# Kernel optimization log

Measured on AMD Instinct MI355X. Metric: run time of the kernel, lower is better.

Reference implementation:

```python
import jax, jax.numpy as jnp
import numpy as np

EMB = 512
H = 8
DK = EMB // H          # 64
MAX_SEQ = 768
TOPK = MAX_SEQ // 2    # 384


def setup_inputs() -> dict:
    key = jax.random.key(0)
    ks = jax.random.split(key, 16)
    B, S, E = 1, MAX_SEQ, EMB

    def w(k, shape):
        return jax.random.normal(k, shape, dtype=jnp.float32) * 0.02

    return {
        "x": jax.random.normal(ks[0], (B, S, E), dtype=jnp.float32),
        # main attention projections (Linear weights stored as (in, out))
        "Wq": w(ks[1], (E, E)), "bq": w(ks[2], (E,)),
        "Wk": w(ks[3], (E, E)), "bk": w(ks[4], (E,)),
        "Wv": w(ks[5], (E, E)), "bv": w(ks[6], (E,)),
        "Wo": w(ks[7], (E, E)), "bo": w(ks[8], (E,)),
        # indexer projections: wq -> (E, H*DK)=(E,E), wk -> (E, DK), weights_proj -> (E, H)
        "iq_W": w(ks[9], (E, H * DK)), "iq_b": w(ks[10], (H * DK,)),
        "ik_W": w(ks[11], (E, DK)),    "ik_b": w(ks[12], (DK,)),
        "wp_W": w(ks[13], (E, H)),     "wp_b": w(ks[14], (H,)),
    }


def reference(x, Wq, bq, Wk, bk, Wv, bv, Wo, bo, iq_W, iq_b, ik_W, ik_b, wp_W, wp_b):
    B, S, E = x.shape
    scaling = 1.0 / np.sqrt(DK)

    def split_heads(z):  # (B,S,E) -> (B,H,S,DK)
        return z.reshape(B, S, H, DK).transpose(0, 2, 1, 3)

    Q = split_heads(x @ Wq + bq)
    K = split_heads(x @ Wk + bk)
    V = split_heads(x @ Wv + bv)

    # --- indexer: per-token relevance scores ---
    q_idx = (x @ iq_W + iq_b).reshape(B, S, H, DK).transpose(0, 2, 1, 3)  # (B,H,S,DK)
    k_idx = x @ ik_W + ik_b                                               # (B,S,DK)
    w_idx = x @ wp_W + wp_b                                               # (B,S,H)
    score = jax.nn.relu(jnp.einsum('bhsd,btd->bhst', q_idx, k_idx))       # (B,H,S,S)
    indexer_score = jnp.einsum('bhst,bsh->bst', score, w_idx)             # (B,S,S)

    # --- top-k selection (set-equivalent to argpartition in the original) ---
    topk_idx = jax.lax.top_k(indexer_score, TOPK)[1]                      # (B,S,TOPK) int32

    # --- gather sparse K/V per query token ---
    def gather_b(Zb, idxb):  # Zb:(H,S,DK), idxb:(S,TOPK) -> (H,S,TOPK,DK)
        return Zb[:, idxb, :]
    K_s = jax.vmap(gather_b)(K, topk_idx)  # (B,H,S,TOPK,DK)
    V_s = jax.vmap(gather_b)(V, topk_idx)  # (B,H,S,TOPK,DK)

    # --- sparse attention over selected tokens ---
    sc = jnp.einsum('bhsd,bhskd->bhsk', Q, K_s) * scaling  # (B,H,S,TOPK)
    wts = jax.nn.softmax(sc, axis=-1)
    attn = jnp.einsum('bhsk,bhskd->bhsd', wts, V_s)        # (B,H,S,DK)

    out = attn.transpose(0, 2, 1, 3).reshape(B, S, E) @ Wo + bo
    return out
```

## Files before the change

kernel.cpp:

```cpp
#include <hip/hip_runtime.h>
#include <hip/hip_bf16.h>
#include <math.h>

#define S 768
#define E 512
#define H 8
#define DK 64
#define TOPK 384

typedef short bf16x8 __attribute__((ext_vector_type(8)));
typedef float f32x4 __attribute__((ext_vector_type(4)));

__device__ __forceinline__ unsigned short f2bf(float x) {
  unsigned u = __float_as_uint(x);
  unsigned r = u + 0x7FFFu + ((u >> 16) & 1u);
  return (unsigned short)(r >> 16);
}
__device__ __forceinline__ float bf2f(unsigned short h) {
  return __uint_as_float(((unsigned)h) << 16);
}
__device__ __forceinline__ void split1(float x, unsigned short& h, unsigned short& l) {
  h = f2bf(x);
  l = f2bf(x - bf2f(h));
}

__device__ __forceinline__ void mfma3(f32x4& d, bf16x8 ah, bf16x8 al,
                                      bf16x8 bh, bf16x8 bl) {
  d = __builtin_amdgcn_mfma_f32_16x16x32_bf16(ah, bh, d, 0, 0, 0);
  d = __builtin_amdgcn_mfma_f32_16x16x32_bf16(ah, bl, d, 0, 0, 0);
  d = __builtin_amdgcn_mfma_f32_16x16x32_bf16(al, bh, d, 0, 0, 0);
}
__device__ __forceinline__ void mfma2(f32x4& d, bf16x8 ah, bf16x8 al, bf16x8 bh) {
  d = __builtin_amdgcn_mfma_f32_16x16x32_bf16(ah, bh, d, 0, 0, 0);
  d = __builtin_amdgcn_mfma_f32_16x16x32_bf16(al, bh, d, 0, 0, 0);
}

__device__ __forceinline__ bf16x8 ldfrag(const unsigned short* p) {
  return *reinterpret_cast<const bf16x8*>(p);
}

struct PrepTab {
  const float* src[8];
  unsigned short* hi[8];
  unsigned short* lo[8];
};

__global__ __launch_bounds__(256) void prep_kernel(PrepTab t) {
  const int seg = blockIdx.z;
  const int rows = (seg == 0) ? 768 : 512;
  const int cols = (seg == 5) ? 64 : ((seg == 6) ? 8 : 512);
  const int tx = (seg == 6) ? 2 : ((cols + 31) >> 5);
  const int ty = rows >> 5;
  if ((int)blockIdx.x >= tx || (int)blockIdx.y >= ty) return;
  const int r0 = blockIdx.y * 32, c0 = blockIdx.x * 32;
  const int tid = threadIdx.x;
  const int rl = tid >> 3, c4 = (tid & 7) << 2;
  const float* src = t.src[seg];
  if (seg == 0) {
    float4 v = *(const float4*)(src + (size_t)(r0 + rl) * cols + c0 + c4);
    unsigned short h[4], l[4];
    split1(v.x, h[0], l[0]); split1(v.y, h[1], l[1]);
    split1(v.z, h[2], l[2]); split1(v.w, h[3], l[3]);
    size_t off = (size_t)(r0 + rl) * cols + c0 + c4;
    *(ushort4*)(t.hi[seg] + off) = make_ushort4(h[0], h[1], h[2], h[3]);
    *(ushort4*)(t.lo[seg] + off) = make_ushort4(l[0], l[1], l[2], l[3]);
  } else {
    __shared__ float ts[32][33];
    #pragma unroll
    for (int j = 0; j < 4; ++j) {
      int c = c4 + j;
      ts[rl][c] = (c0 + c < cols) ? src[(size_t)(r0 + rl) * cols + c0 + c] : 0.0f;
    }
    __syncthreads();
    float v0 = ts[c4 + 0][rl], v1 = ts[c4 + 1][rl];
    float v2 = ts[c4 + 2][rl], v3 = ts[c4 + 3][rl];
    unsigned short h[4], l[4];
    split1(v0, h[0], l[0]); split1(v1, h[1], l[1]);
    split1(v2, h[2], l[2]); split1(v3, h[3], l[3]);
    size_t off = (size_t)(c0 + rl) * 512 + r0 + c4;
    *(ushort4*)(t.hi[seg] + off) = make_ushort4(h[0], h[1], h[2], h[3]);
    *(ushort4*)(t.lo[seg] + off) = make_ushort4(l[0], l[1], l[2], l[3]);
  }
}

struct ProjTab {
  const unsigned short* whi[6];
  const unsigned short* wlo[6];
  const float* bias[6];
};

__global__ __launch_bounds__(256) void proj_mfma_kernel(
    const unsigned short* __restrict__ Xhi, const unsigned short* __restrict__ Xlo,
    ProjTab pt,
    unsigned short* __restrict__ Qhi, unsigned short* __restrict__ Qlo,
    unsigned short* __restrict__ Khi, unsigned short* __restrict__ Klo,
    unsigned short* __restrict__ VThi,
    unsigned short* __restrict__ QIhi, unsigned short* __restrict__ QIlo,
    unsigned short* __restrict__ KIhi, unsigned short* __restrict__ KIlo,
    float* __restrict__ WI) {
  __shared__ __align__(16) unsigned short Ah[64][72];
  __shared__ __align__(16) unsigned short Al[64][72];
  __shared__ __align__(16) unsigned short Bh[64][72];
  __shared__ __align__(16) unsigned short Bl[64][72];
  const int bx = blockIdx.x;
  int seg, nt;
  if (bx < 32) { seg = bx >> 3; nt = bx & 7; }
  else         { seg = 4 + (bx - 32); nt = 0; }
  const int m0 = blockIdx.y * 64;
  const int n0 = nt * 64;
  const int tid = threadIdx.x;
  const int lane = tid & 63;
  const int wave = tid >> 6;
  const int mq = (wave >> 1) << 5;
  const int nq = (wave & 1) << 5;
  const int l15 = lane & 15;
  const int q8 = (lane >> 4) << 3;
  const int q4 = (lane >> 4) << 2;
  const unsigned short* Whi = pt.whi[seg];
  const unsigned short* Wlo = pt.wlo[seg];

  const int mm0 = tid >> 3,          kc0 = (tid & 7) << 3;
  const int mm1 = (tid + 256) >> 3,  kc1 = ((tid + 256) & 7) << 3;
  const size_t ga0 = (size_t)(m0 + mm0) * 512 + kc0;
  const size_t gb0 = (size_t)(n0 + mm0) * 512 + kc0;
  const size_t ga1 = (size_t)(m0 + mm1) * 512 + kc1;
  const size_t gb1 = (size_t)(n0 + mm1) * 512 + kc1;

  bf16x8 rah0 = ldfrag(Xhi + ga0), ral0 = ldfrag(Xlo + ga0);
  bf16x8 rbh0 = ldfrag(Whi + gb0), rbl0 = ldfrag(Wlo + gb0);
  bf16x8 rah1 = ldfrag(Xhi + ga1), ral1 = ldfrag(Xlo + ga1);
  bf16x8 rbh1 = ldfrag(Whi + gb1), rbl1 = ldfrag(Wlo + gb1);

  f32x4 acc[2][2] = {};
  for (int cc = 0; cc < 8; ++cc) {
    *(bf16x8*)&Ah[mm0][kc0] = rah0;
    *(bf16x8*)&Al[mm0][kc0] = ral0;
    *(bf16x8*)&Bh[mm0][kc0] = rbh0;
    *(bf16x8*)&Bl[mm0][kc0] = rbl0;
    *(bf16x8*)&Ah[mm1][kc1] = rah1;
    *(bf16x8*)&Al[mm1][kc1] = ral1;
    *(bf16x8*)&Bh[mm1][kc1] = rbh1;
    *(bf16x8*)&Bl[mm1][kc1] = rbl1;
    if (cc < 7) {
      const size_t o = (size_t)(cc + 1) << 6;
      rah0 = ldfrag(Xhi + ga0 + o); ral0 = ldfrag(Xlo + ga0 + o);
      rbh0 = ldfrag(Whi + gb0 + o); rbl0 = ldfrag(Wlo + gb0 + o);
      rah1 = ldfrag(Xhi + ga1 + o); ral1 = ldfrag(Xlo + ga1 + o);
      rbh1 = ldfrag(Whi + gb1 + o); rbl1 = ldfrag(Wlo + gb1 + o);
    }
    __syncthreads();
    #pragma unroll
    for (int ki = 0; ki < 64; ki += 32) {
      const int kk = ki + q8;
      bf16x8 ah0 = *(const bf16x8*)&Ah[mq + l15][kk];
      bf16x8 al0 = *(const bf16x8*)&Al[mq + l15][kk];
      bf16x8 ah1 = *(const bf16x8*)&Ah[mq + 16 + l15][kk];
      bf16x8 al1 = *(const bf16x8*)&Al[mq + 16 + l15][kk];
      bf16x8 bh0 = *(const bf16x8*)&Bh[nq + l15][kk];
      bf16x8 bl0 = *(const bf16x8*)&Bl[nq + l15][kk];
      bf16x8 bh1 = *(const bf16x8*)&Bh[nq + 16 + l15][kk];
      bf16x8 bl1 = *(const bf16x8*)&Bl[nq + 16 + l15][kk];
      mfma3(acc[0][0], ah0, al0, bh0, bl0);
      mfma3(acc[0][1], ah0, al0, bh1, bl1);
      mfma3(acc[1][0], ah1, al1, bh0, bl0);
      mfma3(acc[1][1], ah1, al1, bh1, bl1);
    }
    __syncthreads();
  }

  const float* bias = pt.bias[seg];
  #pragma unroll
  for (int ntt = 0; ntt < 2; ++ntt) {
    const int nloc = n0 + nq + ntt * 16 + l15;
    const float bv = (seg == 5 && nloc >= 8) ? 0.0f : bias[nloc];
    #pragma unroll
    for (int mt = 0; mt < 2; ++mt) {
      #pragma unroll
      for (int r = 0; r < 4; ++r) {
        const int m = m0 + mq + mt * 16 + q4 + r;
        const float v = acc[mt][ntt][r] + bv;
        unsigned short h16, l16;
        if (seg == 0) {
          split1(v, h16, l16);
          Qhi[(size_t)m * 512 + nloc] = h16;
          Qlo[(size_t)m * 512 + nloc] = l16;
        } else if (seg == 1) {
          const int hh = nloc >> 6, dd = nloc & 63;
          split1(v, h16, l16);
          Khi[((size_t)hh * S + m) * 64 + dd] = h16;
          Klo[((size_t)hh * S + m) * 64 + dd] = l16;
        } else if (seg == 2) {
          VThi[((size_t)(nloc >> 6) * 64 + (nloc & 63)) * S + m] = f2bf(v);
        } else if (seg == 3) {
          split1(v, h16, l16);
          QIhi[(size_t)m * 512 + nloc] = h16;
          QIlo[(size_t)m * 512 + nloc] = l16;
        } else if (seg == 4) {
          split1(v, h16, l16);
          KIhi[(size_t)m * 64 + nloc] = h16;
          KIlo[(size_t)m * 64 + nloc] = l16;
        } else {
          if (nloc < 8) WI[(size_t)m * 8 + nloc] = v;
        }
      }
    }
  }
}

__global__ __launch_bounds__(256) void indexer_mfma_kernel(
    const unsigned short* __restrict__ QIhi, const unsigned short* __restrict__ QIlo,
    const unsigned short* __restrict__ KIhi, const unsigned short* __restrict__ KIlo,
    const float* __restrict__ WI, float* __restrict__ ISC) {
  __shared__ __align__(16) unsigned short Qh[32][136];
  __shared__ __align__(16) unsigned short Ql[32][136];
  __shared__ float wis[32][8];
  const int s0 = blockIdx.y * 32, t0 = blockIdx.x * 64;
  const int tid = threadIdx.x;
  const int lane = tid & 63;
  const int wave = tid >> 6;
  const int mq = (wave >> 1) << 4;
  const int nqb = (wave & 1) << 5;
  const int l15 = lane & 15;
  const int q8 = (lane >> 4) << 3;
  const int q4 = (lane >> 4) << 2;
  wis[tid >> 3][tid & 7] = WI[(size_t)(s0 + (tid >> 3)) * 8 + (tid & 7)];

  const size_t brow0 = (size_t)(t0 + nqb + l15) * 64;
  const size_t brow1 = (size_t)(t0 + nqb + 16 + l15) * 64;
  bf16x8 kfh[2][2], kfl[2][2];
  #pragma unroll
  for (int kk = 0; kk < 2; ++kk) {
    const int kb = kk * 32 + q8;
    kfh[kk][0] = ldfrag(KIhi + brow0 + kb);
    kfl[kk][0] = ldfrag(KIlo + brow0 + kb);
    kfh[kk][1] = ldfrag(KIhi + brow1 + kb);
    kfl[kk][1] = ldfrag(KIlo + brow1 + kb);
  }

  const int smm = tid >> 3;
  const int skc = (tid & 7) << 4;
  const size_t qbase = (size_t)(s0 + smm) * 512 + skc;
  bf16x8 rq0 = ldfrag(QIhi + qbase);
  bf16x8 rq1 = ldfrag(QIhi + qbase + 8);
  bf16x8 rq2 = ldfrag(QIlo + qbase);
  bf16x8 rq3 = ldfrag(QIlo + qbase + 8);

  float accI[2][4] = {};
  for (int hp = 0; hp < 4; ++hp) {
    __syncthreads();
    *(bf16x8*)&Qh[smm][skc]     = rq0;
    *(bf16x8*)&Qh[smm][skc + 8] = rq1;
    *(bf16x8*)&Ql[smm][skc]     = rq2;
    *(bf16x8*)&Ql[smm][skc + 8] = rq3;
    if (hp < 3) {
      const size_t g = qbase + (size_t)(hp + 1) * 128;
      rq0 = ldfrag(QIhi + g);
      rq1 = ldfrag(QIhi + g + 8);
      rq2 = ldfrag(QIlo + g);
      rq3 = ldfrag(QIlo + g + 8);
    }
    __syncthreads();
    #pragma unroll
    for (int hh = 0; hh < 2; ++hh) {
      const int h = hp * 2 + hh;
      f32x4 d[2] = {};
      #pragma unroll
      for (int kk = 0; kk < 2; ++kk) {
        const int ka = hh * 64 + kk * 32 + q8;
        bf16x8 ah = *(const bf16x8*)&Qh[mq + l15][ka];
        bf16x8 al = *(const bf16x8*)&Ql[mq + l15][ka];
        mfma3(d[0], ah, al, kfh[kk][0], kfl[kk][0]);
        mfma3(d[1], ah, al, kfh[kk][1], kfl[kk][1]);
      }
      #pragma unroll
      for (int r = 0; r < 4; ++r) {
        const float w = wis[mq + q4 + r][h];
        accI[0][r] = fmaf(fmaxf(d[0][r], 0.0f), w, accI[0][r]);
        accI[1][r] = fmaf(fmaxf(d[1][r], 0.0f), w, accI[1][r]);
      }
    }
  }
  #pragma unroll
  for (int ntt = 0; ntt < 2; ++ntt)
    #pragma unroll
    for (int r = 0; r < 4; ++r)
      ISC[(size_t)(s0 + mq + q4 + r) * S + t0 + nqb + ntt * 16 + l15] = accI[ntt][r];
}

__global__ __launch_bounds__(256) void topk_kernel(
    const float* __restrict__ ISC, unsigned* __restrict__ Mask,
    float* __restrict__ Sum, float* __restrict__ ATTacc) {
  __shared__ unsigned ordv[768];
  __shared__ int hist[256];
  __shared__ int gsum[16];
  __shared__ int wtot[4];
  __shared__ unsigned mw[24];
  __shared__ unsigned sh_prefix;
  __shared__ int sh_R;
  const int s = blockIdx.x;
  const int tid = threadIdx.x;
  for (int i = tid; i < 768; i += 256) {
    float f = ISC[s * 768 + i] + 0.0f;
    unsigned u = __float_as_uint(f);
    ordv[i] = (u & 0x80000000u) ? ~u : (u | 0x80000000u);
  }
  {
    const float4 z4 = {0.0f, 0.0f, 0.0f, 0.0f};
    if (tid < 128) *(float4*)(ATTacc + (size_t)s * 512 + tid * 4) = z4;
  }
  if (tid < 24) mw[tid] = 0u;
  if (tid < H) Sum[tid * S + s] = 0.0f;
  if (tid == 0) { sh_prefix = 0u; sh_R = TOPK; }
  __syncthreads();
  for (int pass = 0; pass < 4; ++pass) {
    const int shift = 24 - pass * 8;
    hist[tid] = 0;
    __syncthreads();
    const unsigned pm = (pass == 0) ? 0u : (0xFFFFFFFFu << (shift + 8));
    const unsigned pref = sh_prefix;
    for (int i = tid; i < 768; i += 256) {
      unsigned o = ordv[i];
      if ((o & pm) == pref) atomicAdd(&hist[(o >> shift) & 255], 1);
    }
    __syncthreads();
    if (tid < 16) {
      int t = 0;
      #pragma unroll
      for (int k = 0; k < 16; ++k) t += hist[tid * 16 + k];
      gsum[tid] = t;
    }
    __syncthreads();
    if (tid == 0) {
      int R = sh_R;
      int G = 0;
      int g = 15;
      for (; g > 0; --g) {
        if (G + gsum[g] >= R) break;
        G += gsum[g];
      }
      int b = 15;
      for (; b > 0; --b) {
        int c = hist[g * 16 + b];
        if (G + c >= R) break;
        G += c;
      }
      sh_prefix = sh_prefix | ((unsigned)(g * 16 + b) << shift);
      sh_R = R - G;
    }
    __syncthreads();
  }
  const unsigned thr = sh_prefix;
  const int need_eq = sh_R;
  const int base = tid * 3;
  unsigned o0 = ordv[base], o1 = ordv[base + 1], o2 = ordv[base + 2];
  int c = (o0 == thr) + (o1 == thr) + (o2 == thr);
  const int lane = tid & 63, wv = tid >> 6;
  int sum = c;
  #pragma unroll
  for (int off = 1; off < 64; off <<= 1) {
    int v = __shfl_up(sum, off);
    if (lane >= off) sum += v;
  }
  if (lane == 63) wtot[wv] = sum;
  __syncthreads();
  int rank = sum - c;
  if (wv > 0) rank += wtot[0];
  if (wv > 1) rank += wtot[1];
  if (wv > 2) rank += wtot[2];
  if (o0 > thr || (o0 == thr && rank < need_eq))
    atomicOr(&mw[base >> 5], 1u << (base & 31));
  if (o0 == thr) ++rank;
  if (o1 > thr || (o1 == thr && rank < need_eq))
    atomicOr(&mw[(base + 1) >> 5], 1u << ((base + 1) & 31));
  if (o1 == thr) ++rank;
  if (o2 > thr || (o2 == thr && rank < need_eq))
    atomicOr(&mw[(base + 2) >> 5], 1u << ((base + 2) & 31));
  __syncthreads();
  if (tid < 24) Mask[s * 24 + tid] = mw[tid];
}

__global__ __launch_bounds__(512) void sattn_kernel(
    const unsigned short* __restrict__ Qhi, const unsigned short* __restrict__ Qlo,
    const unsigned short* __restrict__ Khi, const unsigned short* __restrict__ Klo,
    const unsigned short* __restrict__ VThi,
    const unsigned* __restrict__ Mask, float* __restrict__ ATTacc,
    float* __restrict__ Sum) {
  __shared__ __align__(16) unsigned short Ksh[64][72];
  __shared__ __align__(16) unsigned short Ksl[64][72];
  __shared__ __align__(16) unsigned short Pshi[64][72];
  __shared__ __align__(16) unsigned short Pslo[64][72];
  __shared__ unsigned msk[64][6];
  __shared__ float rsumf[64];
  const int ks = blockIdx.x;
  const int s0 = blockIdx.y * 64;
  const int h  = blockIdx.z;
  const int tid = threadIdx.x;
  const int lane = tid & 63;
  const int wave = tid >> 6;
  const int l15 = lane & 15;
  const int q8 = (lane >> 4) << 3;
  const int q4 = (lane >> 4) << 2;
  const int mq = (wave >> 1) << 4;
  const int nqq = (wave & 1) << 4;
  const int db = (wave & 1) << 5;

  if (tid < 384) msk[tid & 63][tid >> 6] =
      Mask[(size_t)(s0 + (tid & 63)) * 24 + ks * 6 + (tid >> 6)];
  if (tid < 64) rsumf[tid] = 0.0f;

  const size_t qrow = (size_t)(s0 + mq + l15) * 512 + h * 64;
  bf16x8 qh0 = ldfrag(Qhi + qrow + q8);
  bf16x8 ql0 = ldfrag(Qlo + qrow + q8);
  bf16x8 qh1 = ldfrag(Qhi + qrow + 32 + q8);
  bf16x8 ql1 = ldfrag(Qlo + qrow + 32 + q8);

  const int tr = tid >> 3;
  const int kc = (tid & 7) << 3;
  const size_t gkbase = ((size_t)h * S + ks * 192 + tr) * 64 + kc;
  bf16x8 rkh = ldfrag(Khi + gkbase);
  bf16x8 rkl = ldfrag(Klo + gkbase);

  const size_t vb0 = ((size_t)h * 64 + db + l15) * S + ks * 192 + q8;
  bf16x8 v00 = ldfrag(VThi + vb0);
  bf16x8 v01 = ldfrag(VThi + vb0 + 32);
  bf16x8 v10 = ldfrag(VThi + vb0 + (size_t)16 * S);
  bf16x8 v11 = ldfrag(VThi + vb0 + (size_t)16 * S + 32);

  float esum[4] = {0.0f, 0.0f, 0.0f, 0.0f};
  f32x4 oacc[2] = {};
  for (int ct = 0; ct < 3; ++ct) {
    __syncthreads();
    if (ct > 0) {
      #pragma unroll
      for (int kk = 0; kk < 64; kk += 32) {
        bf16x8 pah = *(const bf16x8*)&Pshi[mq + l15][kk + q8];
        bf16x8 pal = *(const bf16x8*)&Pslo[mq + l15][kk + q8];
        mfma2(oacc[0], pah, pal, (kk == 0) ? v00 : v01);
        mfma2(oacc[1], pah, pal, (kk == 0) ? v10 : v11);
      }
      const size_t vo = vb0 + (size_t)ct * 64;
      v00 = ldfrag(VThi + vo);
      v01 = ldfrag(VThi + vo + 32);
      v10 = ldfrag(VThi + vo + (size_t)16 * S);
      v11 = ldfrag(VThi + vo + (size_t)16 * S + 32);
    }
    *(bf16x8*)&Ksh[tr][kc] = rkh;
    *(bf16x8*)&Ksl[tr][kc] = rkl;
    if (ct < 2) {
      rkh = ldfrag(Khi + gkbase + (size_t)(ct + 1) * 4096);
      rkl = ldfrag(Klo + gkbase + (size_t)(ct + 1) * 4096);
    }
    __syncthreads();
    #pragma unroll
    for (int cp = 0; cp < 2; ++cp) {
      const int tcol = nqq + cp * 32;
      f32x4 d = {0.0f, 0.0f, 0.0f, 0.0f};
      bf16x8 bh0 = *(const bf16x8*)&Ksh[tcol + l15][q8];
      bf16x8 bl0 = *(const bf16x8*)&Ksl[tcol + l15][q8];
      bf16x8 bh1 = *(const bf16x8*)&Ksh[tcol + l15][32 + q8];
      bf16x8 bl1 = *(const bf16x8*)&Ksl[tcol + l15][32 + q8];
      mfma3(d, qh0, ql0, bh0, bl0);
      mfma3(d, qh1, ql1, bh1, bl1);
      const int tl = ct * 64 + tcol + l15;
      #pragma unroll
      for (int r = 0; r < 4; ++r) {
        const int srow = mq + q4 + r;
        const unsigned w = msk[srow][tl >> 5];
        float e = ((w >> (tl & 31)) & 1u) ? __expf(d[r] * 0.125f) : 0.0f;
        unsigned short h16, l16;
        split1(e, h16, l16);
        Pshi[srow][tcol + l15] = h16;
        Pslo[srow][tcol + l15] = l16;
        esum[r] += e;
      }
    }
  }
  __syncthreads();
  #pragma unroll
  for (int kk = 0; kk < 64; kk += 32) {
    bf16x8 pah = *(const bf16x8*)&Pshi[mq + l15][kk + q8];
    bf16x8 pal = *(const bf16x8*)&Pslo[mq + l15][kk + q8];
    mfma2(oacc[0], pah, pal, (kk == 0) ? v00 : v01);
    mfma2(oacc[1], pah, pal, (kk == 0) ? v10 : v11);
  }
  #pragma unroll
  for (int dt = 0; dt < 2; ++dt) {
    const int dd = db + dt * 16 + l15;
    #pragma unroll
    for (int r = 0; r < 4; ++r) {
      const int s = s0 + mq + q4 + r;
      atomicAdd(&ATTacc[(size_t)s * E + h * DK + dd], oacc[dt][r]);
    }
  }
  #pragma unroll
  for (int off = 1; off < 16; off <<= 1) {
    esum[0] += __shfl_xor(esum[0], off);
    esum[1] += __shfl_xor(esum[1], off);
    esum[2] += __shfl_xor(esum[2], off);
    esum[3] += __shfl_xor(esum[3], off);
  }
  if (l15 == 0) {
    atomicAdd(&rsumf[q4 + 0 + mq], esum[0]);
    atomicAdd(&rsumf[q4 + 1 + mq], esum[1]);
    atomicAdd(&rsumf[q4 + 2 + mq], esum[2]);
    atomicAdd(&rsumf[q4 + 3 + mq], esum[3]);
  }
  __syncthreads();
  if (tid < 64) atomicAdd(&Sum[(size_t)h * S + s0 + tid], rsumf[tid]);
}

__global__ __launch_bounds__(512) void out_mfma_kernel(
    const float* __restrict__ ATTacc, const float* __restrict__ Sum,
    const unsigned short* __restrict__ WoThi,
    const float* __restrict__ bo, float* __restrict__ out) {
  __shared__ float AccL[16][65];
  __shared__ float ivs[16][8];
  __shared__ __align__(16) unsigned short Ahi[16][520];
  __shared__ __align__(16) unsigned short Alo[16][520];
  const int tid512 = threadIdx.x;
  const int wave8 = tid512 >> 6;
  const int z = wave8 >> 2;
  const int wave = wave8 & 3;
  const int lane = tid512 & 63;
  const int m0 = blockIdx.y * 16;
  const int n0 = blockIdx.x * 64 + wave * 16;
  const int l15 = lane & 15;
  const int q8 = (lane >> 4) << 3;
  const int q4 = (lane >> 4) << 2;
  if (tid512 < 128) {
    const int r = tid512 >> 3, hh = tid512 & 7;
    ivs[r][hh] = 1.0f / Sum[(size_t)hh * S + m0 + r];
  }
  __syncthreads();
  {
    const int row = tid512 >> 5;
    const int kb = (tid512 & 31) << 4;
    const float inv = ivs[row][kb >> 6];
    const float* src = ATTacc + (size_t)(m0 + row) * 512 + kb;
    float4 a0 = *(const float4*)(src);
    float4 a1 = *(const float4*)(src + 4);
    float4 a2 = *(const float4*)(src + 8);
    float4 a3 = *(const float4*)(src + 12);
    float v[16] = {a0.x, a0.y, a0.z, a0.w, a1.x, a1.y, a1.z, a1.w,
                   a2.x, a2.y, a2.z, a2.w, a3.x, a3.y, a3.z, a3.w};
    #pragma unroll
    for (int i = 0; i < 16; ++i) {
      unsigned short hh, ll;
      split1(v[i] * inv, hh, ll);
      Ahi[row][kb + i] = hh;
      Alo[row][kb + i] = ll;
    }
  }
  __syncthreads();
  const size_t brow = (size_t)(n0 + l15) * 512;
  f32x4 acc = {};
  #pragma unroll
  for (int it = 0; it < 8; ++it) {
    const int ko = (z << 8) + (it << 5) + q8;
    bf16x8 ah = *(const bf16x8*)&Ahi[l15][ko];
    bf16x8 al = *(const bf16x8*)&Alo[l15][ko];
    bf16x8 bh = ldfrag(WoThi + brow + ko);
    mfma2(acc, ah, al, bh);
  }
  if (z == 1) {
    #pragma unroll
    for (int r = 0; r < 4; ++r)
      AccL[q4 + r][wave * 16 + l15] = acc[r];
  }
  __syncthreads();
  if (z == 0) {
    const int n = n0 + l15;
    const float bv = bo[n];
    #pragma unroll
    for (int r = 0; r < 4; ++r)
      out[(size_t)(m0 + q4 + r) * 512 + n] =
          acc[r] + AccL[q4 + r][wave * 16 + l15] + bv;
  }
}

extern "C" void kernel_launch(void* const* d_in, const int* in_sizes, int n_in,
                              void* d_out, int out_size, void* d_ws, size_t ws_size,
                              hipStream_t stream) {
  const float* x    = (const float*)d_in[0];
  const float* Wq   = (const float*)d_in[1];
  const float* bq   = (const float*)d_in[2];
  const float* Wk   = (const float*)d_in[3];
  const float* bk   = (const float*)d_in[4];
  const float* Wv   = (const float*)d_in[5];
  const float* bv   = (const float*)d_in[6];
  const float* Wo   = (const float*)d_in[7];
  const float* bo   = (const float*)d_in[8];
  const float* iqW  = (const float*)d_in[9];
  const float* iqb  = (const float*)d_in[10];
  const float* ikW  = (const float*)d_in[11];
  const float* ikb  = (const float*)d_in[12];
  const float* wpW  = (const float*)d_in[13];
  const float* wpb  = (const float*)d_in[14];

  float* ws = (float*)d_ws;
  float* WI   = ws;
  float* ISC  = WI + S * H;
  unsigned* Mask = (unsigned*)(ISC + S * S);
  float* Sum  = (float*)(Mask + S * 24);
  float* ATTacc = Sum + H * S;
  unsigned short* u = (unsigned short*)(ATTacc + S * E);
  unsigned short* Xhi  = u;             u += S * E;
  unsigned short* Xlo  = u;             u += S * E;
  unsigned short* Qhi  = u;             u += S * E;
  unsigned short* Qlo  = u;             u += S * E;
  unsigned short* Khi  = u;             u += S * E;
  unsigned short* Klo  = u;             u += S * E;
  unsigned short* VThi = u;             u += S * E;
  unsigned short* QIhi = u;             u += S * E;
  unsigned short* QIlo = u;             u += S * E;
  unsigned short* KIhi = u;             u += S * DK;
  unsigned short* KIlo = u;             u += S * DK;
  unsigned short* WTq_hi = u;           u += E * E;
  unsigned short* WTk_hi = u;           u += E * E;
  unsigned short* WTv_hi = u;           u += E * E;
  unsigned short* WTiq_hi = u;          u += E * E;
  unsigned short* WTik_hi = u;          u += 64 * E;
  unsigned short* WTwp_hi = u;          u += 64 * E;
  unsigned short* WTo_hi = u;           u += E * E;
  unsigned short* WTq_lo = u;           u += E * E;
  unsigned short* WTk_lo = u;           u += E * E;
  unsigned short* WTv_lo = u;           u += E * E;
  unsigned short* WTiq_lo = u;          u += E * E;
  unsigned short* WTik_lo = u;          u += 64 * E;
  unsigned short* WTwp_lo = u;          u += 64 * E;
  unsigned short* WTo_lo = u;           u += E * E;

  PrepTab prep;
  prep.src[0] = x;    prep.hi[0] = Xhi;     prep.lo[0] = Xlo;
  prep.src[1] = Wq;   prep.hi[1] = WTq_hi;  prep.lo[1] = WTq_lo;
  prep.src[2] = Wk;   prep.hi[2] = WTk_hi;  prep.lo[2] = WTk_lo;
  prep.src[3] = Wv;   prep.hi[3] = WTv_hi;  prep.lo[3] = WTv_lo;
  prep.src[4] = iqW;  prep.hi[4] = WTiq_hi; prep.lo[4] = WTiq_lo;
  prep.src[5] = ikW;  prep.hi[5] = WTik_hi; prep.lo[5] = WTik_lo;
  prep.src[6] = wpW;  prep.hi[6] = WTwp_hi; prep.lo[6] = WTwp_lo;
  prep.src[7] = Wo;   prep.hi[7] = WTo_hi;  prep.lo[7] = WTo_lo;

  ProjTab pt;
  pt.whi[0] = WTq_hi;  pt.wlo[0] = WTq_lo;  pt.bias[0] = bq;
  pt.whi[1] = WTk_hi;  pt.wlo[1] = WTk_lo;  pt.bias[1] = bk;
  pt.whi[2] = WTv_hi;  pt.wlo[2] = WTv_lo;  pt.bias[2] = bv;
  pt.whi[3] = WTiq_hi; pt.wlo[3] = WTiq_lo; pt.bias[3] = iqb;
  pt.whi[4] = WTik_hi; pt.wlo[4] = WTik_lo; pt.bias[4] = ikb;
  pt.whi[5] = WTwp_hi; pt.wlo[5] = WTwp_lo; pt.bias[5] = wpb;

  prep_kernel<<<dim3(16, 24, 8), dim3(256), 0, stream>>>(prep);
  proj_mfma_kernel<<<dim3(34, S / 64), dim3(256), 0, stream>>>(
      Xhi, Xlo, pt, Qhi, Qlo, Khi, Klo, VThi, QIhi, QIlo, KIhi, KIlo, WI);
  indexer_mfma_kernel<<<dim3(S / 64, S / 32), dim3(256), 0, stream>>>(
      QIhi, QIlo, KIhi, KIlo, WI, ISC);
  topk_kernel<<<dim3(S), dim3(256), 0, stream>>>(ISC, Mask, Sum, ATTacc);
  sattn_kernel<<<dim3(4, S / 64, H), dim3(512), 0, stream>>>(
      Qhi, Qlo, Khi, Klo, VThi, Mask, ATTacc, Sum);
  out_mfma_kernel<<<dim3(8, 48), dim3(512), 0, stream>>>(
      ATTacc, Sum, WTo_hi, bo, (float*)d_out);
}
```

Baseline: 138.1 us.

## Double block sizes in projection and indexer kernels to share tiles

The projection GEMM now uses 512-thread blocks covering 128 rows of X per block. This halves the number of blocks that load each weight tile, since one 64-row B tile now serves twice as many rows. The indexer kernel packs two 32-row query halves into one 512-thread block, each half with its own shared buffers, which halves the grid. The aim is to reuse weight and key fragments more and cut launch and block overhead. The cost is fewer blocks (about 204 in the projection) on a GPU with many CUs, so occupancy and load balance may suffer.

Result: slower. 141.1 us (+2.2%).

```diff
diff --git a/kernel.cpp b/kernel.cpp
--- a/kernel.cpp
+++ b/kernel.cpp
@@ -89,7 +89,7 @@
   const float* bias[6];
 };
 
-__global__ __launch_bounds__(256) void proj_mfma_kernel(
+__global__ __launch_bounds__(512) void proj_mfma_kernel(
     const unsigned short* __restrict__ Xhi, const unsigned short* __restrict__ Xlo,
     ProjTab pt,
     unsigned short* __restrict__ Qhi, unsigned short* __restrict__ Qlo,
@@ -98,15 +98,15 @@
     unsigned short* __restrict__ QIhi, unsigned short* __restrict__ QIlo,
     unsigned short* __restrict__ KIhi, unsigned short* __restrict__ KIlo,
     float* __restrict__ WI) {
-  __shared__ __align__(16) unsigned short Ah[64][72];
-  __shared__ __align__(16) unsigned short Al[64][72];
+  __shared__ __align__(16) unsigned short Ah[128][72];
+  __shared__ __align__(16) unsigned short Al[128][72];
   __shared__ __align__(16) unsigned short Bh[64][72];
   __shared__ __align__(16) unsigned short Bl[64][72];
   const int bx = blockIdx.x;
   int seg, nt;
   if (bx < 32) { seg = bx >> 3; nt = bx & 7; }
   else         { seg = 4 + (bx - 32); nt = 0; }
-  const int m0 = blockIdx.y * 64;
+  const int m0 = blockIdx.y * 128;
   const int n0 = nt * 64;
   const int tid = threadIdx.x;
   const int lane = tid & 63;
@@ -119,34 +119,30 @@
   const unsigned short* Whi = pt.whi[seg];
   const unsigned short* Wlo = pt.wlo[seg];
 
-  const int mm0 = tid >> 3,          kc0 = (tid & 7) << 3;
-  const int mm1 = (tid + 256) >> 3,  kc1 = ((tid + 256) & 7) << 3;
-  const size_t ga0 = (size_t)(m0 + mm0) * 512 + kc0;
-  const size_t gb0 = (size_t)(n0 + mm0) * 512 + kc0;
-  const size_t ga1 = (size_t)(m0 + mm1) * 512 + kc1;
-  const size_t gb1 = (size_t)(n0 + mm1) * 512 + kc1;
+  const int amm0 = tid >> 3;
+  const int amm1 = amm0 + 64;
+  const int kcs  = (tid & 7) << 3;
+  const size_t ga0 = (size_t)(m0 + amm0) * 512 + kcs;
+  const size_t ga1 = (size_t)(m0 + amm1) * 512 + kcs;
+  const size_t gb  = (size_t)(n0 + amm0) * 512 + kcs;
 
   bf16x8 rah0 = ldfrag(Xhi + ga0), ral0 = ldfrag(Xlo + ga0);
-  bf16x8 rbh0 = ldfrag(Whi + gb0), rbl0 = ldfrag(Wlo + gb0);
   bf16x8 rah1 = ldfrag(Xhi + ga1), ral1 = ldfrag(Xlo + ga1);
-  bf16x8 rbh1 = ldfrag(Whi + gb1), rbl1 = ldfrag(Wlo + gb1);
+  bf16x8 rbh  = ldfrag(Whi + gb),  rbl  = ldfrag(Wlo + gb);
 
   f32x4 acc[2][2] = {};
   for (int cc = 0; cc < 8; ++cc) {
-    *(bf16x8*)&Ah[mm0][kc0] = rah0;
-    *(bf16x8*)&Al[mm0][kc0] = ral0;
-    *(bf16x8*)&Bh[mm0][kc0] = rbh0;
-    *(bf16x8*)&Bl[mm0][kc0] = rbl0;
-    *(bf16x8*)&Ah[mm1][kc1] = rah1;
-    *(bf16x8*)&Al[mm1][kc1] = ral1;
-    *(bf16x8*)&Bh[mm1][kc1] = rbh1;
-    *(bf16x8*)&Bl[mm1][kc1] = rbl1;
+    *(bf16x8*)&Ah[amm0][kcs] = rah0;
+    *(bf16x8*)&Al[amm0][kcs] = ral0;
+    *(bf16x8*)&Ah[amm1][kcs] = rah1;
+    *(bf16x8*)&Al[amm1][kcs] = ral1;
+    *(bf16x8*)&Bh[amm0][kcs] = rbh;
+    *(bf16x8*)&Bl[amm0][kcs] = rbl;
     if (cc < 7) {
       const size_t o = (size_t)(cc + 1) << 6;
       rah0 = ldfrag(Xhi + ga0 + o); ral0 = ldfrag(Xlo + ga0 + o);
-      rbh0 = ldfrag(Whi + gb0 + o); rbl0 = ldfrag(Wlo + gb0 + o);
       rah1 = ldfrag(Xhi + ga1 + o); ral1 = ldfrag(Xlo + ga1 + o);
-      rbh1 = ldfrag(Whi + gb1 + o); rbl1 = ldfrag(Wlo + gb1 + o);
+      rbh  = ldfrag(Whi + gb + o);  rbl  = ldfrag(Wlo + gb + o);
     }
     __syncthreads();
     #pragma unroll
@@ -207,15 +203,17 @@
   }
 }
 
-__global__ __launch_bounds__(256) void indexer_mfma_kernel(
+__global__ __launch_bounds__(512) void indexer_mfma_kernel(
     const unsigned short* __restrict__ QIhi, const unsigned short* __restrict__ QIlo,
     const unsigned short* __restrict__ KIhi, const unsigned short* __restrict__ KIlo,
     const float* __restrict__ WI, float* __restrict__ ISC) {
-  __shared__ __align__(16) unsigned short Qh[32][136];
-  __shared__ __align__(16) unsigned short Ql[32][136];
-  __shared__ float wis[32][8];
-  const int s0 = blockIdx.y * 32, t0 = blockIdx.x * 64;
-  const int tid = threadIdx.x;
+  __shared__ __align__(16) unsigned short Qh[2][32][136];
+  __shared__ __align__(16) unsigned short Ql[2][32][136];
+  __shared__ float wis[2][32][8];
+  const int half = threadIdx.x >> 8;
+  const int tid = threadIdx.x & 255;
+  const int s0 = blockIdx.y * 64 + half * 32;
+  const int t0 = blockIdx.x * 64;
   const int lane = tid & 63;
   const int wave = tid >> 6;
   const int mq = (wave >> 1) << 4;
@@ -223,7 +221,7 @@
   const int l15 = lane & 15;
   const int q8 = (lane >> 4) << 3;
   const int q4 = (lane >> 4) << 2;
-  wis[tid >> 3][tid & 7] = WI[(size_t)(s0 + (tid >> 3)) * 8 + (tid & 7)];
+  wis[half][tid >> 3][tid & 7] = WI[(size_t)(s0 + (tid >> 3)) * 8 + (tid & 7)];
 
   const size_t brow0 = (size_t)(t0 + nqb + l15) * 64;
   const size_t brow1 = (size_t)(t0 + nqb + 16 + l15) * 64;
@@ -248,10 +246,10 @@
   float accI[2][4] = {};
   for (int hp = 0; hp < 4; ++hp) {
     __syncthreads();
-    *(bf16x8*)&Qh[smm][skc]     = rq0;
-    *(bf16x8*)&Qh[smm][skc + 8] = rq1;
-    *(bf16x8*)&Ql[smm][skc]     = rq2;
-    *(bf16x8*)&Ql[smm][skc + 8] = rq3;
+    *(bf16x8*)&Qh[half][smm][skc]     = rq0;
+    *(bf16x8*)&Qh[half][smm][skc + 8] = rq1;
+    *(bf16x8*)&Ql[half][smm][skc]     = rq2;
+    *(bf16x8*)&Ql[half][smm][skc + 8] = rq3;
     if (hp < 3) {
       const size_t g = qbase + (size_t)(hp + 1) * 128;
       rq0 = ldfrag(QIhi + g);
@@ -267,14 +265,14 @@
       #pragma unroll
       for (int kk = 0; kk < 2; ++kk) {
         const int ka = hh * 64 + kk * 32 + q8;
-        bf16x8 ah = *(const bf16x8*)&Qh[mq + l15][ka];
-        bf16x8 al = *(const bf16x8*)&Ql[mq + l15][ka];
+        bf16x8 ah = *(const bf16x8*)&Qh[half][mq + l15][ka];
+        bf16x8 al = *(const bf16x8*)&Ql[half][mq + l15][ka];
         mfma3(d[0], ah, al, kfh[kk][0], kfl[kk][0]);
         mfma3(d[1], ah, al, kfh[kk][1], kfl[kk][1]);
       }
       #pragma unroll
       for (int r = 0; r < 4; ++r) {
-        const float w = wis[mq + q4 + r][h];
+        const float w = wis[half][mq + q4 + r][h];
         accI[0][r] = fmaf(fmaxf(d[0][r], 0.0f), w, accI[0][r]);
         accI[1][r] = fmaf(fmaxf(d[1][r], 0.0f), w, accI[1][r]);
       }
@@ -649,9 +647,9 @@
   pt.whi[5] = WTwp_hi; pt.wlo[5] = WTwp_lo; pt.bias[5] = wpb;
 
   prep_kernel<<<dim3(16, 24, 8), dim3(256), 0, stream>>>(prep);
-  proj_mfma_kernel<<<dim3(34, S / 64), dim3(256), 0, stream>>>(
+  proj_mfma_kernel<<<dim3(34, S / 128), dim3(512), 0, stream>>>(
       Xhi, Xlo, pt, Qhi, Qlo, Khi, Klo, VThi, QIhi, QIlo, KIhi, KIlo, WI);
-  indexer_mfma_kernel<<<dim3(S / 64, S / 32), dim3(256), 0, stream>>>(
+  indexer_mfma_kernel<<<dim3(S / 64, S / 64), dim3(512), 0, stream>>>(
       QIhi, QIlo, KIhi, KIlo, WI, ISC);
   topk_kernel<<<dim3(S), dim3(256), 0, stream>>>(ISC, Mask, Sum, ATTacc);
   sattn_kernel<<<dim3(4, S / 64, H), dim3(512), 0, stream>>>(
```
